# Kernel optimization log

Hardware: AMD Instinct MI355X
Metric: run time of the kernel (lower is better)

## Reference

```python
import jax, jax.numpy as jnp
import numpy as np

N, D, L, K = 250000, 16, 6, 64
COST_GAMMA = 0.1
MIN_ZERO_GAMMA = 0.1
EPS = 1e-7  # clip for arccos numerical stability


def setup_inputs() -> dict:
    key = jax.random.key(0)
    k1, k2, k3, k4 = jax.random.split(key, 4)
    xs = jax.random.normal(k1, (N, D), jnp.float32)
    xs = xs / jnp.linalg.norm(xs, axis=1, keepdims=True)  # points on sphere S^{D-1}
    mus = jax.random.normal(k2, (L, D, K), jnp.float32)    # per-layer component locations
    alphas = jax.random.uniform(k3, (L, K), jnp.float32, minval=-1.0, maxval=1.0)
    ws = jax.random.uniform(k4, (L,), jnp.float32, minval=0.0, maxval=1.0)
    return {"xs": xs, "mus": mus, "alphas": alphas, "ws": ws}


def reference(xs, mus, alphas, ws):
    # projx: normalize each mu column onto the sphere (norm over D axis)
    mu_n = mus / jnp.linalg.norm(mus, axis=1, keepdims=True)          # [L, D, K]
    # sphere cost: 0.5 * geodesic_dist^2 = 0.5 * arccos(<x, mu>)^2
    inner = jnp.einsum('nd,ldk->lnk', xs, mu_n)                        # [L, N, K]
    dist = jnp.arccos(jnp.clip(inner, -1.0 + EPS, 1.0 - EPS))
    costs = 0.5 * dist * dist + alphas[:, None, :]                     # [L, N, K]
    # soft-min over components (note sign convention follows original: +gamma*LSE(-c/gamma))
    mincosts = COST_GAMMA * jax.nn.logsumexp(-costs / COST_GAMMA, axis=2)  # [L, N]
    wv = jnp.exp(-ws ** 2)                                             # [L]
    F = jnp.zeros((xs.shape[0],), xs.dtype)
    for i in range(L):  # small fixed layer recurrence
        F = wv[i] * jax.nn.relu(F) + (1.0 - wv[i]) * mincosts[i]
    # smooth min(F, 0): gamma * LSE(-[F,0]/gamma)
    Fz = jnp.stack((F, jnp.zeros_like(F)), axis=-1)
    F = MIN_ZERO_GAMMA * jax.nn.logsumexp(-Fz / MIN_ZERO_GAMMA, axis=-1)
    return F
```

## Files before the change

kernel.cpp:

```cpp
#include <hip/hip_runtime.h>
#include <math.h>

#define NPOINTS 250000
#define LL 6
#define DD 16
#define KK 64

#define TPB 256
#define WAVES_PER_BLOCK (TPB / 64)
#define PTS_PER_WAVE 16
#define PTS_PER_BLOCK (WAVES_PER_BLOCK * PTS_PER_WAVE)

#define LDS_BYTES (WAVES_PER_BLOCK * PTS_PER_WAVE * 80)

#define WS_MU 0
#define WS_AV 24576
#define WS_WV 26112

typedef __attribute__((ext_vector_type(8))) short bf16x8;
typedef __attribute__((ext_vector_type(4))) float f32x4;
typedef __attribute__((ext_vector_type(2))) float f32x2;

#if __has_builtin(__builtin_amdgcn_exp2f)
#define EXP2F(x) __builtin_amdgcn_exp2f(x)
#else
#define EXP2F(x) exp2f(x)
#endif
#if __has_builtin(__builtin_amdgcn_logf)
#define LOG2F(x) __builtin_amdgcn_logf(x)
#else
#define LOG2F(x) log2f(x)
#endif

#define C_AA   (-14.426950408889634f)
#define C_GLN2 (0.06931471805599453f)

#define W0  17.797117f
#define VT0 (-45.300328f)
#define VT1 (-28.559404f)
#define VT2 (-27.844414f)
#define VT3 (-30.475230f)
#define VT4 (-36.246253f)
#define VT5 (-27.207285f)

__device__ __forceinline__ f32x2 s2(float v) { f32x2 r; r.x = v; r.y = v; return r; }

__device__ __forceinline__ ushort bf16_rne(float f) {
  unsigned u = __float_as_uint(f);
  unsigned r = u + 0x7FFFu + ((u >> 16) & 1u);
  return (ushort)(r >> 16);
}

__device__ __forceinline__ f32x2 term2(f32x2 xp, f32x2 aaw) {
  f32x2 x2  = xp * xp;
  f32x2 p01 = __builtin_elementwise_fma(s2(VT1), xp, s2(VT0));
  f32x2 p23 = __builtin_elementwise_fma(s2(VT3), xp, s2(VT2));
  f32x2 p45 = __builtin_elementwise_fma(s2(VT5), xp, s2(VT4));
  f32x2 qq  = __builtin_elementwise_fma(x2, p45, p23);
  f32x2 V   = __builtin_elementwise_fma(x2, qq, p01);
  f32x2 t2  = __builtin_elementwise_fma(xp, V, aaw);
  f32x2 e; e.x = EXP2F(t2.x); e.y = EXP2F(t2.y);
  return e;
}

__global__ __launch_bounds__(384) void
prep_kernel(const float* __restrict__ mus,
            const float* __restrict__ alphas,
            const float* __restrict__ wsv,
            char* __restrict__ ws) {
  const int t = threadIdx.x;
  const float* colp = mus + (t >> 6) * (DD * KK) + (t & 63);
  float v[DD];
  float ss = 0.0f;
#pragma unroll
  for (int d = 0; d < DD; ++d) { v[d] = colp[d * KK]; ss = fmaf(v[d], v[d], ss); }
  float inv = -0.5f / sqrtf(ss);
  unsigned hw[8], lw[8];
#pragma unroll
  for (int i = 0; i < 8; ++i) {
    float a0 = v[2 * i] * inv;
    float a1 = v[2 * i + 1] * inv;
    ushort h0 = bf16_rne(a0), h1 = bf16_rne(a1);
    float hf0 = __uint_as_float((unsigned)h0 << 16);
    float hf1 = __uint_as_float((unsigned)h1 << 16);
    ushort l0 = bf16_rne(a0 - hf0), l1 = bf16_rne(a1 - hf1);
    hw[i] = (unsigned)h0 | ((unsigned)h1 << 16);
    lw[i] = (unsigned)l0 | ((unsigned)l1 << 16);
  }
  uint4* colq = (uint4*)(ws + WS_MU + t * 64);
  colq[0] = make_uint4(hw[0], hw[1], hw[2], hw[3]);
  colq[1] = make_uint4(hw[4], hw[5], hw[6], hw[7]);
  colq[2] = make_uint4(lw[0], lw[1], lw[2], lw[3]);
  colq[3] = make_uint4(lw[4], lw[5], lw[6], lw[7]);
  ((float*)(ws + WS_AV))[t] = fmaf(C_AA, alphas[t], -W0);
  if (t < LL) { float x = wsv[t]; ((float*)(ws + WS_WV))[t] = expf(-x * x); }
}

__global__ __launch_bounds__(TPB, 4) void
multiinf_kernel(const float* __restrict__ xs,
                const char* __restrict__ ws,
                float* __restrict__ out) {
  __shared__ __align__(16) char smem[LDS_BYTES];

  const int tid = threadIdx.x;
  const int wid = tid >> 6;
  const int lane = tid & 63;
  const int c = lane & 15;
  const int q = lane >> 4;
  const int h = q & 1;
  const int pt0 = blockIdx.x * PTS_PER_BLOCK + wid * PTS_PER_WAVE;
  char* sx = smem + wid * (PTS_PER_WAVE * 80);

  {
    int gidx = pt0 + c;
    float4 a = make_float4(0.0f, 0.0f, 0.0f, 0.0f);
    if (gidx < NPOINTS) a = ((const float4*)(xs + (size_t)gidx * DD))[q];
    ushort h0 = bf16_rne(a.x), h1 = bf16_rne(a.y);
    ushort h2 = bf16_rne(a.z), h3 = bf16_rne(a.w);
    float hf0 = __uint_as_float((unsigned)h0 << 16);
    float hf1 = __uint_as_float((unsigned)h1 << 16);
    float hf2 = __uint_as_float((unsigned)h2 << 16);
    float hf3 = __uint_as_float((unsigned)h3 << 16);
    ushort l0 = bf16_rne(a.x - hf0), l1 = bf16_rne(a.y - hf1);
    ushort l2 = bf16_rne(a.z - hf2), l3 = bf16_rne(a.w - hf3);
    uint2 hwv, lwv;
    hwv.x = (unsigned)h0 | ((unsigned)h1 << 16);
    hwv.y = (unsigned)h2 | ((unsigned)h3 << 16);
    lwv.x = (unsigned)l0 | ((unsigned)l1 << 16);
    lwv.y = (unsigned)l2 | ((unsigned)l3 << 16);
    *(uint2*)(sx + c * 80 + q * 8) = hwv;
    *(uint2*)(sx + c * 80 + 32 + q * 8) = lwv;
  }

  bf16x8 Bh = *(const bf16x8*)(sx + c * 80 + h * 16);
  bf16x8 Bl = *(const bf16x8*)(sx + c * 80 + 32 + h * 16);

  const float* swv = (const float*)(ws + WS_WV);
  const f32x4 zero4 = {0.0f, 0.0f, 0.0f, 0.0f};
  float F = 0.0f;

#pragma unroll 2
  for (int l = 0; l < LL; ++l) {
    bf16x8 Am[4];
    f32x2 aaL[4], aaH[4];
#pragma unroll
    for (int cb = 0; cb < 4; ++cb) {
      Am[cb] = *(const bf16x8*)(ws + WS_MU + (l * 64 + cb * 16 + c) * 64 + q * 16);
      f32x4 a4 = *(const f32x4*)(ws + WS_AV + (l * 64 + cb * 16 + q * 4) * 4);
      aaL[cb].x = a4.x; aaL[cb].y = a4.y;
      aaH[cb].x = a4.z; aaH[cb].y = a4.w;
    }
    f32x2 S01 = s2(0.0f), S23 = s2(0.0f);
#pragma unroll
    for (int cb = 0; cb < 4; ++cb) {
      f32x4 acc = __builtin_amdgcn_mfma_f32_16x16x32_bf16(Am[cb], Bh, zero4, 0, 0, 0);
      acc = __builtin_amdgcn_mfma_f32_16x16x32_bf16(Am[cb], Bl, acc, 0, 0, 0);
      f32x2 a01; a01.x = acc[0]; a01.y = acc[1];
      f32x2 a23; a23.x = acc[2]; a23.y = acc[3];
      S01 += term2(a01, aaL[cb]);
      S23 += term2(a23, aaH[cb]);
    }
    f32x2 Sf = S01 + S23;
    float St = Sf.x + Sf.y;
    St += __shfl_xor(St, 16, 64);
    St += __shfl_xor(St, 32, 64);
    float wvl = swv[l];
    float mc = C_GLN2 * LOG2F(St);
    F = fmaf(wvl, fmaxf(F, 0.0f), (1.0f - wvl) * mc);
  }

  if (lane < 16) {
    int idx = pt0 + c;
    if (idx < NPOINTS) {
      float e = EXP2F(F * C_AA);
      out[idx] = C_GLN2 * LOG2F(1.0f + e);
    }
  }
}

extern "C" void kernel_launch(void* const* d_in, const int* in_sizes, int n_in,
                              void* d_out, int out_size, void* d_ws, size_t ws_size,
                              hipStream_t stream) {
  const float* xs = (const float*)d_in[0];
  const float* mus = (const float*)d_in[1];
  const float* alphas = (const float*)d_in[2];
  const float* wsv = (const float*)d_in[3];
  float* out = (float*)d_out;
  char* ws = (char*)d_ws;
  (void)ws_size;

  prep_kernel<<<1, 384, 0, stream>>>(mus, alphas, wsv, ws);
  const int blocks = (NPOINTS + PTS_PER_BLOCK - 1) / PTS_PER_BLOCK;
  multiinf_kernel<<<blocks, TPB, 0, stream>>>(xs, ws, out);
}
```

Before: 102.1 us.

## Process four point tiles per wave, reusing mu fragments and double-buffering layer loads

Each wave now handles 64 points as four 16-point MFMA tiles instead of one, so each loaded mu fragment and alpha vector is reused across four B operands. Mu loads for the next layer are double-buffered ahead of the current layer's compute, and the exp2 calls are batched after the polynomial evaluation to expose more ILP. Block size drops to 128 threads with a lower occupancy hint, trading fewer waves and more registers per thread for less redundant global/L2 traffic and better latency hiding. The final output is written by all 64 lanes, each selecting its tile's F.

```diff
diff --git a/kernel.cpp b/kernel.cpp
--- a/kernel.cpp
+++ b/kernel.cpp
@@ -6,9 +6,9 @@
 #define DD 16
 #define KK 64
 
-#define TPB 256
+#define TPB 128
 #define WAVES_PER_BLOCK (TPB / 64)
-#define PTS_PER_WAVE 16
+#define PTS_PER_WAVE 64
 #define PTS_PER_BLOCK (WAVES_PER_BLOCK * PTS_PER_WAVE)
 
 #define LDS_BYTES (WAVES_PER_BLOCK * PTS_PER_WAVE * 80)
@@ -51,16 +51,32 @@
   return (ushort)(r >> 16);
 }
 
-__device__ __forceinline__ f32x2 term2(f32x2 xp, f32x2 aaw) {
+__device__ __forceinline__ f32x2 poly_t2(f32x2 xp, f32x2 aaw) {
   f32x2 x2  = xp * xp;
   f32x2 p01 = __builtin_elementwise_fma(s2(VT1), xp, s2(VT0));
   f32x2 p23 = __builtin_elementwise_fma(s2(VT3), xp, s2(VT2));
   f32x2 p45 = __builtin_elementwise_fma(s2(VT5), xp, s2(VT4));
   f32x2 qq  = __builtin_elementwise_fma(x2, p45, p23);
   f32x2 V   = __builtin_elementwise_fma(x2, qq, p01);
-  f32x2 t2  = __builtin_elementwise_fma(xp, V, aaw);
-  f32x2 e; e.x = EXP2F(t2.x); e.y = EXP2F(t2.y);
-  return e;
+  return __builtin_elementwise_fma(xp, V, aaw);
+}
+
+__device__ __forceinline__ void pack_pt(char* dst, float4 a, int q) {
+  ushort h0 = bf16_rne(a.x), h1 = bf16_rne(a.y);
+  ushort h2 = bf16_rne(a.z), h3 = bf16_rne(a.w);
+  float hf0 = __uint_as_float((unsigned)h0 << 16);
+  float hf1 = __uint_as_float((unsigned)h1 << 16);
+  float hf2 = __uint_as_float((unsigned)h2 << 16);
+  float hf3 = __uint_as_float((unsigned)h3 << 16);
+  ushort l0 = bf16_rne(a.x - hf0), l1 = bf16_rne(a.y - hf1);
+  ushort l2 = bf16_rne(a.z - hf2), l3 = bf16_rne(a.w - hf3);
+  uint2 hwv, lwv;
+  hwv.x = (unsigned)h0 | ((unsigned)h1 << 16);
+  hwv.y = (unsigned)h2 | ((unsigned)h3 << 16);
+  lwv.x = (unsigned)l0 | ((unsigned)l1 << 16);
+  lwv.y = (unsigned)l2 | ((unsigned)l3 << 16);
+  *(uint2*)(dst + q * 8) = hwv;
+  *(uint2*)(dst + 32 + q * 8) = lwv;
 }
 
 __global__ __launch_bounds__(384) void
@@ -96,7 +112,7 @@
   if (t < LL) { float x = wsv[t]; ((float*)(ws + WS_WV))[t] = expf(-x * x); }
 }
 
-__global__ __launch_bounds__(TPB, 4) void
+__global__ __launch_bounds__(TPB, 3) void
 multiinf_kernel(const float* __restrict__ xs,
                 const char* __restrict__ ws,
                 float* __restrict__ out) {
@@ -111,68 +127,98 @@
   const int pt0 = blockIdx.x * PTS_PER_BLOCK + wid * PTS_PER_WAVE;
   char* sx = smem + wid * (PTS_PER_WAVE * 80);
 
-  {
-    int gidx = pt0 + c;
+#pragma unroll
+  for (int t = 0; t < 4; ++t) {
+    int p = pt0 + 16 * t + c;
     float4 a = make_float4(0.0f, 0.0f, 0.0f, 0.0f);
-    if (gidx < NPOINTS) a = ((const float4*)(xs + (size_t)gidx * DD))[q];
-    ushort h0 = bf16_rne(a.x), h1 = bf16_rne(a.y);
-    ushort h2 = bf16_rne(a.z), h3 = bf16_rne(a.w);
-    float hf0 = __uint_as_float((unsigned)h0 << 16);
-    float hf1 = __uint_as_float((unsigned)h1 << 16);
-    float hf2 = __uint_as_float((unsigned)h2 << 16);
-    float hf3 = __uint_as_float((unsigned)h3 << 16);
-    ushort l0 = bf16_rne(a.x - hf0), l1 = bf16_rne(a.y - hf1);
-    ushort l2 = bf16_rne(a.z - hf2), l3 = bf16_rne(a.w - hf3);
-    uint2 hwv, lwv;
-    hwv.x = (unsigned)h0 | ((unsigned)h1 << 16);
-    hwv.y = (unsigned)h2 | ((unsigned)h3 << 16);
-    lwv.x = (unsigned)l0 | ((unsigned)l1 << 16);
-    lwv.y = (unsigned)l2 | ((unsigned)l3 << 16);
-    *(uint2*)(sx + c * 80 + q * 8) = hwv;
-    *(uint2*)(sx + c * 80 + 32 + q * 8) = lwv;
-  }
-
-  bf16x8 Bh = *(const bf16x8*)(sx + c * 80 + h * 16);
-  bf16x8 Bl = *(const bf16x8*)(sx + c * 80 + 32 + h * 16);
+    if (p < NPOINTS) a = ((const float4*)(xs + (size_t)p * DD))[q];
+    pack_pt(sx + (16 * t + c) * 80, a, q);
+  }
+
+  bf16x8 Bh[4], Bl[4];
+#pragma unroll
+  for (int t = 0; t < 4; ++t) {
+    Bh[t] = *(const bf16x8*)(sx + (16 * t + c) * 80 + h * 16);
+    Bl[t] = *(const bf16x8*)(sx + (16 * t + c) * 80 + 32 + h * 16);
+  }
 
   const float* swv = (const float*)(ws + WS_WV);
   const f32x4 zero4 = {0.0f, 0.0f, 0.0f, 0.0f};
-  float F = 0.0f;
-
-#pragma unroll 2
-  for (int l = 0; l < LL; ++l) {
-    bf16x8 Am[4];
-    f32x2 aaL[4], aaH[4];
+  float F[4] = {0.0f, 0.0f, 0.0f, 0.0f};
+
+  auto load_Am = [&](int l, bf16x8* Am) {
+#pragma unroll
+    for (int cb = 0; cb < 4; ++cb)
+      Am[cb] = *(const bf16x8*)(ws + WS_MU + (l * 64 + cb * 16 + c) * 64 + q * 16);
+  };
+  auto load_aa = [&](int l, f32x2* aaL, f32x2* aaH) {
 #pragma unroll
     for (int cb = 0; cb < 4; ++cb) {
-      Am[cb] = *(const bf16x8*)(ws + WS_MU + (l * 64 + cb * 16 + c) * 64 + q * 16);
       f32x4 a4 = *(const f32x4*)(ws + WS_AV + (l * 64 + cb * 16 + q * 4) * 4);
       aaL[cb].x = a4.x; aaL[cb].y = a4.y;
       aaH[cb].x = a4.z; aaH[cb].y = a4.w;
     }
-    f32x2 S01 = s2(0.0f), S23 = s2(0.0f);
+  };
+
+  auto layer_body = [&](int l, const bf16x8* Am) {
+    f32x2 aaL[4], aaH[4];
+    load_aa(l, aaL, aaH);
+    f32x2 S[8];
+#pragma unroll
+    for (int i = 0; i < 8; ++i) S[i] = s2(0.0f);
 #pragma unroll
     for (int cb = 0; cb < 4; ++cb) {
-      f32x4 acc = __builtin_amdgcn_mfma_f32_16x16x32_bf16(Am[cb], Bh, zero4, 0, 0, 0);
-      acc = __builtin_amdgcn_mfma_f32_16x16x32_bf16(Am[cb], Bl, acc, 0, 0, 0);
-      f32x2 a01; a01.x = acc[0]; a01.y = acc[1];
-      f32x2 a23; a23.x = acc[2]; a23.y = acc[3];
-      S01 += term2(a01, aaL[cb]);
-      S23 += term2(a23, aaH[cb]);
-    }
-    f32x2 Sf = S01 + S23;
-    float St = Sf.x + Sf.y;
-    St += __shfl_xor(St, 16, 64);
-    St += __shfl_xor(St, 32, 64);
+      f32x4 acc[4];
+#pragma unroll
+      for (int t = 0; t < 4; ++t) {
+        acc[t] = __builtin_amdgcn_mfma_f32_16x16x32_bf16(Am[cb], Bh[t], zero4, 0, 0, 0);
+        acc[t] = __builtin_amdgcn_mfma_f32_16x16x32_bf16(Am[cb], Bl[t], acc[t], 0, 0, 0);
+      }
+      f32x2 t2[8];
+#pragma unroll
+      for (int t = 0; t < 4; ++t) {
+        f32x2 x01, x23;
+        x01.x = acc[t][0]; x01.y = acc[t][1];
+        x23.x = acc[t][2]; x23.y = acc[t][3];
+        t2[2 * t]     = poly_t2(x01, aaL[cb]);
+        t2[2 * t + 1] = poly_t2(x23, aaH[cb]);
+      }
+      f32x2 e[8];
+#pragma unroll
+      for (int i = 0; i < 8; ++i) { e[i].x = EXP2F(t2[i].x); e[i].y = EXP2F(t2[i].y); }
+#pragma unroll
+      for (int i = 0; i < 8; ++i) S[i] += e[i];
+    }
     float wvl = swv[l];
-    float mc = C_GLN2 * LOG2F(St);
-    F = fmaf(wvl, fmaxf(F, 0.0f), (1.0f - wvl) * mc);
-  }
-
-  if (lane < 16) {
-    int idx = pt0 + c;
+    float om = 1.0f - wvl;
+#pragma unroll
+    for (int t = 0; t < 4; ++t) {
+      f32x2 Sf = S[2 * t] + S[2 * t + 1];
+      float St = Sf.x + Sf.y;
+      St += __shfl_xor(St, 16, 64);
+      St += __shfl_xor(St, 32, 64);
+      float mc = C_GLN2 * LOG2F(St);
+      F[t] = fmaf(wvl, fmaxf(F[t], 0.0f), om * mc);
+    }
+  };
+
+  bf16x8 AmA[4], AmB[4];
+  load_Am(0, AmA);
+#pragma unroll 1
+  for (int lp = 0; lp < 3; ++lp) {
+    int l0 = 2 * lp, l1 = 2 * lp + 1;
+    load_Am(l1, AmB);
+    layer_body(l0, AmA);
+    if (l1 + 1 < LL) load_Am(l1 + 1, AmA);
+    layer_body(l1, AmB);
+  }
+
+  {
+    int t = lane >> 4;
+    float Fv = (t == 0) ? F[0] : (t == 1) ? F[1] : (t == 2) ? F[2] : F[3];
+    int idx = pt0 + lane;
     if (idx < NPOINTS) {
-      float e = EXP2F(F * C_AA);
+      float e = EXP2F(Fv * C_AA);
       out[idx] = C_GLN2 * LOG2F(1.0f + e);
     }
   }
```

New measurement: 95.61 us. -6.4%, faster.
